# Kernel tuning notes

Measured on AMD Instinct MI355X. Metric: run time of the kernel, lower is better.

Reference implementation:

```python
import jax, jax.numpy as jnp
import numpy as np

IMG_H, IMG_W = 800, 1216
STRIDES = [4, 8, 16, 32, 64]
SIZES = [32, 64, 128, 256, 512]
RATIOS = (2.0, 1.0, 0.5)
LVTOP = 1000     # per-level top-k
IMTOP = 1000     # image-level top-k
IOU_THR = 0.7
MIN_SIZE = 0.001
BBOX_CLIP = float(np.log(1000.0 / 16.0))  # dw/dh clamp, matches decode=(1,1,log(1000/16))


def conv2d(x, w, b, pad):
    y = jax.lax.conv_general_dilated(x, w, (1, 1), [(pad, pad), (pad, pad)],
                                     dimension_numbers=('NCHW', 'OIHW', 'NCHW'))
    return y + b[None, :, None, None]


def head_level(x, conv_w, conv_b, cls_w, cls_b, reg_w, reg_b):
    # ConvUnit 3x3 + plain ReLU (no BN), then 1x1 reg/cls heads
    B = x.shape[0]
    h = jax.nn.relu(conv2d(x, conv_w, conv_b, 1))
    reg = conv2d(h, reg_w, reg_b, 0).transpose(0, 2, 3, 1).reshape(B, -1, 4)      # [B,H*W*A,4]
    scr = jax.nn.sigmoid(conv2d(h, cls_w, cls_b, 0).transpose(0, 2, 3, 1).reshape(B, -1))  # [B,H*W*A]
    return reg, scr


def make_priors(H, W, stride, size):
    # rounded base anchors (1 scale x 3 ratios), corner-aligned grid (xyxy)
    r = jnp.array(RATIOS, dtype=jnp.float32)
    hr = jnp.sqrt(r)
    ws, hs = size / hr, size * hr
    base = jnp.round(jnp.stack([-ws / 2, -hs / 2, ws / 2, hs / 2], axis=1))  # [A,4]
    ys, xs = jnp.meshgrid(jnp.arange(H) * stride, jnp.arange(W) * stride, indexing='ij')
    shift = jnp.stack([xs, ys, xs, ys], -1).reshape(-1, 1, 4).astype(jnp.float32)
    return (shift + base[None]).reshape(-1, 4)  # [H*W*A,4], order matches head reshape


def decode(reg, priors):
    pw = priors[..., 2] - priors[..., 0]
    ph = priors[..., 3] - priors[..., 1]
    pcx = priors[..., 0] + 0.5 * pw
    pcy = priors[..., 1] + 0.5 * ph
    dx, dy = reg[..., 0], reg[..., 1]
    dw = jnp.minimum(reg[..., 2], BBOX_CLIP)
    dh = jnp.minimum(reg[..., 3], BBOX_CLIP)
    cx, cy = dx * pw + pcx, dy * ph + pcy
    w, h = jnp.exp(dw) * pw, jnp.exp(dh) * ph
    return jnp.stack([cx - 0.5 * w, cy - 0.5 * h, cx + 0.5 * w, cy + 0.5 * h], -1)


def nms_keep(boxes, scores):
    # greedy NMS; boxes [K,4] sorted by score desc, scores < -0.5 mark invalid/padding
    K = boxes.shape[0]
    area = (boxes[:, 2] - boxes[:, 0]) * (boxes[:, 3] - boxes[:, 1])
    lt = jnp.maximum(boxes[:, None, :2], boxes[None, :, :2])
    rb = jnp.minimum(boxes[:, None, 2:], boxes[None, :, 2:])
    wh = jnp.clip(rb - lt, 0.0)
    inter = wh[..., 0] * wh[..., 1]
    iou = inter / jnp.maximum(area[:, None] + area[None, :] - inter, 1e-9)
    iou = jax.lax.stop_gradient(iou)  # selection is discrete
    idx = jnp.arange(K)

    def step(keep, xs):
        row, i = xs
        sup = keep[i] & (row > IOU_THR) & (idx > i)
        return keep & ~sup, None

    keep, _ = jax.lax.scan(step, scores > -0.5, (iou, idx))
    return keep


def process_level(reg, scr, priors):
    B, N = scr.shape
    k = min(LVTOP, N)
    topv, topi = jax.lax.top_k(scr, k)                              # [B,k], sorted desc
    reg_s = jnp.take_along_axis(reg, topi[..., None], axis=1)       # [B,k,4]
    boxes = decode(reg_s, priors[topi])
    boxes = jnp.stack([
        jnp.clip(boxes[..., 0], 0.0, IMG_W), jnp.clip(boxes[..., 1], 0.0, IMG_H),
        jnp.clip(boxes[..., 2], 0.0, IMG_W), jnp.clip(boxes[..., 3], 0.0, IMG_H)], -1)
    w = boxes[..., 2] - boxes[..., 0]
    h = boxes[..., 3] - boxes[..., 1]
    sc = jnp.where((w > MIN_SIZE) & (h > MIN_SIZE), topv, -1.0)     # drop tiny boxes
    if k < LVTOP:  # pad small levels (e.g. P6) to a fixed candidate count
        boxes = jnp.pad(boxes, ((0, 0), (0, LVTOP - k), (0, 0)))
        sc = jnp.pad(sc, ((0, 0), (0, LVTOP - k)), constant_values=-1.0)
    keep = jax.vmap(nms_keep)(boxes, sc)                            # per-level NMS
    return boxes, jnp.where(keep, sc, -1.0)


def forward(p2, p3, p4, p5, p6, conv_w, conv_b, cls_w, cls_b, reg_w, reg_b):
    levels = [p2, p3, p4, p5, p6]
    all_boxes, all_scores = [], []
    for lvl, stride, size in zip(levels, STRIDES, SIZES):
        reg, scr = head_level(lvl, conv_w, conv_b, cls_w, cls_b, reg_w, reg_b)
        priors = make_priors(lvl.shape[2], lvl.shape[3], stride, size)
        b, s = process_level(reg, scr, priors)
        all_boxes.append(b)
        all_scores.append(s)
    boxes = jnp.concatenate(all_boxes, axis=1)
    scores = jnp.concatenate(all_scores, axis=1)
    fv, fi = jax.lax.top_k(scores, IMTOP)                           # image-level top-k
    fb = jnp.take_along_axis(boxes, fi[..., None], axis=1)
    return jnp.concatenate([fb, fv[..., None]], axis=-1)            # [B, IMTOP, 5]


def setup_inputs():
    key = jax.random.key(0)
    ks = jax.random.split(key, 8)
    C = 256
    shapes = [(2, C, 200, 304), (2, C, 100, 152), (2, C, 50, 76), (2, C, 25, 38), (2, C, 13, 19)]
    inp = {}
    for i, (name, sh) in enumerate(zip(['p2', 'p3', 'p4', 'p5', 'p6'], shapes)):
        inp[name] = jax.random.normal(ks[i], sh, dtype=jnp.float32)
    inp['conv_w'] = jax.random.normal(ks[5], (C, C, 3, 3), dtype=jnp.float32) * 0.02
    inp['conv_b'] = jnp.zeros((C,), dtype=jnp.float32)
    inp['cls_w'] = jax.random.normal(ks[6], (3, C, 1, 1), dtype=jnp.float32) * 0.02
    inp['cls_b'] = jnp.zeros((3,), dtype=jnp.float32)
    inp['reg_w'] = jax.random.normal(ks[7], (12, C, 1, 1), dtype=jnp.float32) * 0.01
    inp['reg_b'] = jnp.zeros((12,), dtype=jnp.float32)
    return inp


def reference(p2, p3, p4, p5, p6, conv_w, conv_b, cls_w, cls_b, reg_w, reg_b):
    return forward(p2, p3, p4, p5, p6, conv_w, conv_b, cls_w, cls_b, reg_w, reg_b)
```

## Files before the change

### kernel.cpp

```cpp
#include <hip/hip_runtime.h>
#include <stdint.h>
#include <math.h>

typedef unsigned long long u64;
typedef unsigned int u32;
typedef unsigned char u8;
typedef short s16x8 __attribute__((ext_vector_type(8)));
typedef float f32x4 __attribute__((ext_vector_type(4)));

#define ATOT 242991
#define PXTOT 80997
#define PXPAD 82971

__device__ __constant__ int    d_Hs[5]      = {200,100,50,25,13};
__device__ __constant__ int    d_Ws[5]      = {304,152,76,38,19};
__device__ __constant__ int    d_Wp[5]      = {306,154,78,40,21};
__device__ __constant__ int    d_stridec[5] = {4,8,16,32,64};
__device__ __constant__ double d_sized[5]   = {32.0,64.0,128.0,256.0,512.0};
__device__ __constant__ int    d_off[5]     = {0,182400,228000,239400,242250};
__device__ __constant__ int    d_pxoff[6]   = {0,60800,76000,79800,80750,80997};
__device__ __constant__ int    d_poff[5]    = {0,61812,77520,81576,82656};
__device__ __constant__ int    d_Ncand[5]   = {182400,45600,11400,2850,741};
__device__ __constant__ int    d_xcb[5]     = {0,1900,2375,2494,2524};
__device__ __constant__ int    d_ctb[5]     = {0,1000,1300,1400,1425};
__device__ __constant__ int    d_tX[5]      = {5,3,2,1,1};
__device__ __constant__ int    d_bcum[6]    = {0,1012,1520,1776,1906,1974};

__device__ __forceinline__ u32 f2k32(float f) {
  u32 u = __float_as_uint(f);
  return (u & 0x80000000u) ? ~u : (u | 0x80000000u);
}
__device__ __forceinline__ float k2f32(u32 k) {
  u32 u = (k & 0x80000000u) ? (k & 0x7FFFFFFFu) : ~k;
  return __uint_as_float(u);
}
__device__ __forceinline__ u64 d2k(double d) {
  u64 b = (u64)__double_as_longlong(d);
  return (b & 0x8000000000000000ull) ? ~b : (b | 0x8000000000000000ull);
}
__device__ __forceinline__ unsigned short f2bf(float v) {
  u32 b = __float_as_uint(v);
  return (unsigned short)((b + 0x7FFFu + ((b >> 16) & 1u)) >> 16);
}

__global__ void wtrans_k(const float* __restrict__ w, float* __restrict__ wt) {
  int gid = blockIdx.x * 256 + threadIdx.x;
  if (gid >= 2304 * 256) return;
  int oc = gid & 255;
  int rest = gid >> 8;
  int ic = rest / 9, tap = rest % 9;
  wt[gid] = w[(oc * 256 + ic) * 9 + tap];
}

__global__ void wcvt_k(const float* __restrict__ w, short* __restrict__ wbh) {
  int gid = blockIdx.x * 256 + threadIdx.x;
  if (gid >= 73728) return;
  int lane = gid & 63;
  int rest = gid >> 6;
  int oct = rest & 15, rs = rest >> 4;
  int slice = rs & 7, tap = rs >> 3;
  int oc = oct * 16 + (lane & 15);
  int icb = slice * 32 + (lane >> 4) * 8;
  size_t ob = (size_t)gid * 8;
#pragma unroll
  for (int j = 0; j < 8; ++j)
    wbh[ob + j] = (short)f2bf(w[(oc * 256 + icb + j) * 9 + tap]);
}

__global__ void border_zero_k(short* __restrict__ xh, short* __restrict__ xl) {
  int tid = blockIdx.x * 256 + threadIdx.x;
  if (tid >= 2 * 1974 * 8) return;
  int oct = tid & 7;
  int rest = tid >> 3;
  int b = rest / 1974;
  int bi = rest % 1974;
  int lvl = 0;
#pragma unroll
  for (int l = 1; l < 5; ++l) if (bi >= d_bcum[l]) lvl = l;
  int li = bi - d_bcum[lvl];
  int W = d_Ws[lvl], H = d_Hs[lvl], Wp = d_Wp[lvl];
  int py, px;
  if (li < Wp)            { py = 0;     px = li; }
  else if (li < 2 * Wp)   { py = H + 1; px = li - Wp; }
  else { int rem = li - 2 * Wp; py = 1 + rem / 2; px = (rem & 1) ? (W + 1) : 0; }
  size_t base = ((size_t)(b * PXPAD + d_poff[lvl]) + (size_t)py * Wp + px) * 256
              + (size_t)oct * 32;
  s16x8 z = (s16x8){0,0,0,0,0,0,0,0};
#pragma unroll
  for (int j = 0; j < 4; ++j) {
    *(s16x8*)(xh + base + j * 8) = z;
    *(s16x8*)(xl + base + j * 8) = z;
  }
}

__global__ __launch_bounds__(256) void xcvt_k(
    const float* __restrict__ x0, const float* __restrict__ x1,
    const float* __restrict__ x2, const float* __restrict__ x3,
    const float* __restrict__ x4, short* __restrict__ xh, short* __restrict__ xl)
{
  __shared__ float tile[32 * 257];
  const int bid = blockIdx.x;
  const int b = bid / 2532;
  int r = bid % 2532;
  int lvl = 0;
#pragma unroll
  for (int l2 = 1; l2 < 5; ++l2) if (r >= d_xcb[l2]) lvl = l2;
  const int chunk = r - d_xcb[lvl];
  const int H = d_Hs[lvl], W = d_Ws[lvl], HW = H * W, Wp = d_Wp[lvl];
  const int px0 = chunk * 32;
  const float* xs[5] = {x0, x1, x2, x3, x4};
  const float* xb = xs[lvl] + (size_t)b * 256 * HW;
  const int t = threadIdx.x;

  for (int icg = 0; icg < 32; ++icg) {
    int ic = icg * 8 + (t >> 5);
    int px = px0 + (t & 31);
    float v = (px < HW) ? xb[(size_t)ic * HW + px] : 0.f;
    tile[(t & 31) * 257 + ic] = v;
  }
  __syncthreads();
  int px = t >> 3, sub = t & 7;
  int gpx = px0 + px;
  if (gpx < HW) {
    int yy = gpx / W, xx = gpx % W;
    size_t pxbase = ((size_t)(b * PXPAD + d_poff[lvl]) +
                     (size_t)(yy + 1) * Wp + (xx + 1)) * 256;
#pragma unroll
    for (int q = 0; q < 4; ++q) {
      int ch0 = q * 64 + sub * 8;
      s16x8 hi, lo;
#pragma unroll
      for (int j = 0; j < 8; ++j) {
        u32 bits = __float_as_uint(tile[px * 257 + ch0 + j]);
        hi[j] = (short)(bits >> 16);
        lo[j] = (short)(bits & 0xFFFFu);
      }
      *(s16x8*)(xh + pxbase + ch0) = hi;
      *(s16x8*)(xl + pxbase + ch0) = lo;
    }
  }
}

__global__ __launch_bounds__(256) void conv_mfma_k(
    const short* __restrict__ xh, const short* __restrict__ wbh,
    const float* __restrict__ convb, const float* __restrict__ clsw,
    const float* __restrict__ clsb, float* __restrict__ scr32)
{
  __shared__ float zl[4][64][3];
  const int bid = blockIdx.x;
  const int b = bid / 1438;
  int r = bid % 1438;
  int lvl = 0;
#pragma unroll
  for (int l2 = 1; l2 < 5; ++l2) if (r >= d_ctb[l2]) lvl = l2;
  const int lid = r - d_ctb[lvl];
  const int tX = d_tX[lvl];
  const int y = lid / tX, x0 = (lid % tX) * 64;
  const int W = d_Ws[lvl], Wp = d_Wp[lvl];
  const size_t pbase = (size_t)(b * PXPAD + d_poff[lvl]);

  const int t = threadIdx.x;
  const int lane = t & 63;
  const int wid = t >> 6;
  const int aoff = (lane & 15) * 256 + (lane >> 4) * 8;

  f32x4 acc[4][4];
#pragma unroll
  for (int m = 0; m < 4; ++m)
#pragma unroll
    for (int o = 0; o < 4; ++o) acc[m][o] = (f32x4){0.f, 0.f, 0.f, 0.f};

#pragma unroll 1
  for (int tap = 0; tap < 9; ++tap) {
    const int ky = tap / 3, kx = tap % 3;
    const size_t re = (pbase + (size_t)(y + ky) * Wp + (x0 + kx)) * 256;
    const short* pa = xh + re;
    const short* pbh = wbh + (size_t)tap * 8 * 16 * 512;
#pragma unroll 1
    for (int slice = 0; slice < 8; ++slice) {
      s16x8 bh[4], a[4];
#pragma unroll
      for (int o = 0; o < 4; ++o) {
        size_t bo = ((size_t)(slice * 16 + wid * 4 + o) * 64 + lane) * 8;
        bh[o] = *(const s16x8*)(pbh + bo);
      }
#pragma unroll
      for (int m = 0; m < 4; ++m) {
        size_t ao = (size_t)aoff + slice * 32 + m * 4096;
        a[m] = *(const s16x8*)(pa + ao);
      }
#pragma unroll
      for (int m = 0; m < 4; ++m)
#pragma unroll
        for (int o = 0; o < 4; ++o)
          acc[m][o] = __builtin_amdgcn_mfma_f32_16x16x32_bf16(a[m], bh[o], acc[m][o], 0, 0, 0);
    }
  }

  float bb[4], cw0[4], cw1[4], cw2[4];
#pragma unroll
  for (int o = 0; o < 4; ++o) {
    int oc = wid * 64 + o * 16 + (lane & 15);
    bb[o]  = convb[oc];
    cw0[o] = clsw[0 * 256 + oc];
    cw1[o] = clsw[1 * 256 + oc];
    cw2[o] = clsw[2 * 256 + oc];
  }
#pragma unroll
  for (int m = 0; m < 4; ++m) {
#pragma unroll
    for (int q = 0; q < 4; ++q) {
      float h0 = fmaxf(acc[m][0][q] + bb[0], 0.f);
      float h1 = fmaxf(acc[m][1][q] + bb[1], 0.f);
      float h2 = fmaxf(acc[m][2][q] + bb[2], 0.f);
      float h3 = fmaxf(acc[m][3][q] + bb[3], 0.f);
      float z0 = fmaf(h0, cw0[0], fmaf(h1, cw0[1], fmaf(h2, cw0[2], h3 * cw0[3])));
      float z1 = fmaf(h0, cw1[0], fmaf(h1, cw1[1], fmaf(h2, cw1[2], h3 * cw1[3])));
      float z2 = fmaf(h0, cw2[0], fmaf(h1, cw2[1], fmaf(h2, cw2[2], h3 * cw2[3])));
      z0 += __shfl_xor(z0, 1); z0 += __shfl_xor(z0, 2); z0 += __shfl_xor(z0, 4); z0 += __shfl_xor(z0, 8);
      z1 += __shfl_xor(z1, 1); z1 += __shfl_xor(z1, 2); z1 += __shfl_xor(z1, 4); z1 += __shfl_xor(z1, 8);
      z2 += __shfl_xor(z2, 1); z2 += __shfl_xor(z2, 2); z2 += __shfl_xor(z2, 4); z2 += __shfl_xor(z2, 8);
      if ((lane & 15) == 0) {
        int slot = m * 16 + (lane >> 4) * 4 + q;
        zl[wid][slot][0] = z0; zl[wid][slot][1] = z1; zl[wid][slot][2] = z2;
      }
    }
  }
  __syncthreads();
  if (t < 192) {
    int slot = t / 3, head = t % 3;
    int col = x0 + slot;
    if (col < W) {
      float z = zl[0][slot][head] + zl[1][slot][head] + zl[2][slot][head] +
                zl[3][slot][head] + clsb[head];
      int pix = y * W + col;
      scr32[(size_t)b * ATOT + d_off[lvl] + (size_t)pix * 3 + head] =
          1.f / (1.f + expf(-z));
    }
  }
}

__device__ __forceinline__ void locate(int gid, int& b, int& r, int& lvl) {
  b = gid / ATOT; r = gid % ATOT;
  lvl = (r < 182400) ? 0 : (r < 228000) ? 1 : (r < 239400) ? 2 : (r < 242250) ? 3 : 4;
}

__global__ void hist_hi_k(const float* __restrict__ scr, u32* __restrict__ hist) {
  int gid = blockIdx.x * 256 + threadIdx.x;
  if (gid >= 2 * ATOT) return;
  int b, r, lvl; locate(gid, b, r, lvl);
  u32 key = f2k32(scr[gid]);
  int rep = blockIdx.x & 3;
  atomicAdd(&hist[((((b * 5 + lvl) << 2) | rep) << 16) + (key >> 16)], 1u);
}

__global__ void scan_hi_k(const u32* __restrict__ hist, int* __restrict__ meta) {
  int bl = blockIdx.x, lvl = bl % 5;
  u32 k_sel = (u32)min(1000, d_Ncand[lvl]);
  const u32* h = hist + ((size_t)bl << 18);
  __shared__ u32 part[256];
  __shared__ u32 row[256];
  __shared__ int csel;
  __shared__ u32 cumsh;
  int t = threadIdx.x;
  u32 s = 0;
  for (int v = 0; v < 256; ++v) {
    int idx = t * 256 + v;
    s += h[idx] + h[65536 + idx] + h[131072 + idx] + h[196608 + idx];
  }
  part[t] = s;
  __syncthreads();
  if (t == 0) {
    u32 cum = 0; int c = 255;
    for (; c > 0; --c) { if (cum + part[c] >= k_sel) break; cum += part[c]; }
    csel = c; cumsh = cum;
  }
  __syncthreads();
  {
    int idx = csel * 256 + t;
    row[t] = h[idx] + h[65536 + idx] + h[131072 + idx] + h[196608 + idx];
  }
  __syncthreads();
  if (t == 0) {
    u32 cum = cumsh;
    int pivot = csel * 256;
    for (int v = 255; v >= 0; --v) {
      if (cum + row[v] >= k_sel) { pivot = csel * 256 + v; break; }
      cum += row[v];
    }
    meta[bl * 8 + 0] = pivot;
    meta[bl * 8 + 1] = (int)cum;
  }
}

__global__ void hist_lo_k(const float* __restrict__ scr, const int* __restrict__ meta,
                          u32* __restrict__ hist) {
  int gid = blockIdx.x * 256 + threadIdx.x;
  if (gid >= 2 * ATOT) return;
  int b, r, lvl; locate(gid, b, r, lvl);
  int bl = b * 5 + lvl;
  u32 key = f2k32(scr[gid]);
  if ((int)(key >> 16) == meta[bl * 8 + 0]) {
    int rep = blockIdx.x & 3;
    atomicAdd(&hist[(((bl << 2) | rep) << 16) + (key & 0xFFFFu)], 1u);
  }
}

__global__ void scan_lo_k(const u32* __restrict__ hist, int* __restrict__ meta) {
  int bl = blockIdx.x, lvl = bl % 5;
  u32 k_sel = (u32)min(1000, d_Ncand[lvl]);
  const u32* h = hist + ((size_t)bl << 18);
  __shared__ u32 part[256];
  __shared__ u32 row[256];
  __shared__ int csel;
  __shared__ u32 cumsh;
  int t = threadIdx.x;
  u32 s = 0;
  for (int v = 0; v < 256; ++v) {
    int idx = t * 256 + v;
    s += h[idx] + h[65536 + idx] + h[131072 + idx] + h[196608 + idx];
  }
  part[t] = s;
  __syncthreads();
  if (t == 0) {
    u32 cum = (u32)meta[bl * 8 + 1];
    int c = 255;
    for (; c > 0; --c) { if (cum + part[c] >= k_sel) break; cum += part[c]; }
    csel = c; cumsh = cum;
  }
  __syncthreads();
  {
    int idx = csel * 256 + t;
    row[t] = h[idx] + h[65536 + idx] + h[131072 + idx] + h[196608 + idx];
  }
  __syncthreads();
  if (t == 0) {
    u32 cum = cumsh;
    int pivot = csel * 256;
    for (int v = 255; v >= 0; --v) {
      if (cum + row[v] >= k_sel) { pivot = csel * 256 + v; break; }
      cum += row[v];
    }
    u32 P = (((u32)meta[bl * 8 + 0]) << 16) | (u32)pivot;
    u32 T = f2k32(k2f32(P) - 5e-3f);
    if (d_Ncand[lvl] <= 1000) T = 0;
    meta[bl * 8 + 2] = (int)T;
    meta[bl * 8 + 4] = 0;
  }
}

__global__ void compact_k(const float* __restrict__ scr, int* __restrict__ meta,
                          u32* __restrict__ complist, u8* __restrict__ flags) {
  int gid = blockIdx.x * 256 + threadIdx.x;
  if (gid >= 2 * ATOT) return;
  int b, r, lvl; locate(gid, b, r, lvl);
  int bl = b * 5 + lvl;
  u32 key = f2k32(scr[gid]);
  if (key >= (u32)meta[bl * 8 + 2]) {
    int pos = atomicAdd(&meta[bl * 8 + 4], 1);
    if (pos < 8192) {
      u32 li = (u32)(r - d_off[lvl]);
      complist[bl * 8192 + pos] = li;
      flags[b * PXTOT + d_pxoff[lvl] + li / 3] = 1;
    }
  }
}

__global__ void pxcompact_k(u8* __restrict__ flags, u32* __restrict__ worklist,
                            int* __restrict__ wlcount) {
  int gid = blockIdx.x * 256 + threadIdx.x;
  if (gid >= 2 * PXTOT) return;
  if (flags[gid]) {
    flags[gid] = 0;
    int pos = atomicAdd(wlcount, 1);
    if (pos < 65536) worklist[pos] = (u32)gid;
  }
}

#define RSG 2048
#define RSLOTS 3
__global__ __launch_bounds__(256) void rescore_k(
    const short* __restrict__ xh, const short* __restrict__ xl,
    const float* __restrict__ wt, const float* __restrict__ convb,
    const float* __restrict__ clsw, const float* __restrict__ clsb,
    const float* __restrict__ regw, const float* __restrict__ regb,
    const u32* __restrict__ worklist, const int* __restrict__ wlcount,
    double* __restrict__ scr64, double* __restrict__ reg64)
{
  __shared__ double xd[RSLOTS * 2560];
  __shared__ double hl[RSLOTS * 256];
  const int t = threadIdx.x;
  int count = *wlcount; if (count > 65536) count = 65536;

  for (int base = blockIdx.x * RSLOTS; base < count; base += RSG * RSLOTS) {
    int sb[RSLOTS], slvl[RSLOTS], spix[RSLOTS];
    size_t pb0[RSLOTS];
    bool valid[RSLOTS];
#pragma unroll
    for (int s = 0; s < RSLOTS; ++s) {
      int w = base + s;
      valid[s] = (w < count);
      sb[s] = 0; slvl[s] = 0; spix[s] = 0; pb0[s] = 0;
      if (valid[s]) {
        u32 g = worklist[w];
        int b = (int)(g / PXTOT), lp = (int)(g % PXTOT);
        int lvl = 0;
#pragma unroll
        for (int l = 1; l < 5; ++l) if (lp >= d_pxoff[l]) lvl = l;
        int pix = lp - d_pxoff[lvl];
        int W = d_Ws[lvl], Wp = d_Wp[lvl];
        int py = pix / W, px = pix % W;
        sb[s] = b; slvl[s] = lvl; spix[s] = pix;
        pb0[s] = ((size_t)(b * PXPAD + d_poff[lvl]) + (size_t)py * Wp + px) * 256;
      }
    }
    __syncthreads();
#pragma unroll
    for (int s = 0; s < RSLOTS; ++s) {
      if (valid[s]) {
        int Wp = d_Wp[slvl[s]];
        for (int i = t; i < 1152; i += 256) {
          int tap = i >> 7, pair = i & 127;
          int ky = tap / 3, kx = tap % 3;
          size_t po = pb0[s] + ((size_t)ky * Wp + kx) * 256 + (size_t)pair * 2;
          u32 vh = *(const u32*)(xh + po);
          u32 vl = *(const u32*)(xl + po);
          float xa  = __uint_as_float(((vh & 0xFFFFu) << 16) | (vl & 0xFFFFu));
          float xb2 = __uint_as_float((vh & 0xFFFF0000u) | (vl >> 16));
          xd[s * 2560 + (pair * 2) * 10 + tap]     = (double)xa;
          xd[s * 2560 + (pair * 2 + 1) * 10 + tap] = (double)xb2;
        }
      }
    }
    __syncthreads();
    double h[RSLOTS];
#pragma unroll
    for (int s = 0; s < RSLOTS; ++s) h[s] = 0.0;
    for (int ic = 0; ic < 256; ++ic) {
      double wd[9];
#pragma unroll
      for (int tap = 0; tap < 9; ++tap)
        wd[tap] = (double)wt[(ic * 9 + tap) * 256 + t];
#pragma unroll
      for (int s = 0; s < RSLOTS; ++s) {
        const double* xp = &xd[s * 2560 + ic * 10];
#pragma unroll
        for (int tap = 0; tap < 9; ++tap)
          h[s] = fma(xp[tap], wd[tap], h[s]);
      }
    }
    double bias = (double)convb[t];
#pragma unroll
    for (int s = 0; s < RSLOTS; ++s) {
      h[s] = fmax(h[s] + bias, 0.0);
      hl[s * 256 + t] = h[s];
    }
    __syncthreads();
    {
      int s = t >> 6, lane = t & 63;
      if (s < RSLOTS && valid[s]) {
        int lvl = slvl[s];
        size_t g3 = (size_t)sb[s] * ATOT + d_off[lvl] + (size_t)spix[s] * 3;
        for (int head = 0; head < 15; ++head) {
          const float* hw = (head < 3) ? (clsw + head * 256) : (regw + (head - 3) * 256);
          double part = 0.0;
#pragma unroll
          for (int q = 0; q < 4; ++q) {
            int oc = lane + q * 64;
            part = fma(hl[s * 256 + oc], (double)hw[oc], part);
          }
          part += __shfl_xor(part, 32);
          part += __shfl_xor(part, 16);
          part += __shfl_xor(part, 8);
          part += __shfl_xor(part, 4);
          part += __shfl_xor(part, 2);
          part += __shfl_xor(part, 1);
          if (lane == 0) {
            double z = part + (double)((head < 3) ? clsb[head] : regb[head - 3]);
            if (head < 3) scr64[g3 + head] = 1.0 / (1.0 + exp(-z));
            else { int hh = head - 3; reg64[(g3 + (hh >> 2)) * 4 + (hh & 3)] = z; }
          }
        }
      }
    }
    __syncthreads();
  }
}

__global__ void buildkeys_k(const u32* __restrict__ complist, const int* __restrict__ meta,
                            const double* __restrict__ scr64, u64* __restrict__ comp64) {
  int bl = blockIdx.x;
  int b = bl / 5, lvl = bl % 5;
  int M = meta[bl * 8 + 4]; if (M > 8192) M = 8192;
  for (int i = threadIdx.x; i < 8192; i += 256) {
    u64 key = 0;
    if (i < M) {
      u32 li = complist[bl * 8192 + i];
      double sc = scr64[(size_t)b * ATOT + d_off[lvl] + li];
      key = ((d2k(sc) >> 18) << 18) | (u64)(0x3FFFFu - li);
    }
    comp64[bl * 8192 + i] = key;
  }
}

__device__ void bitonic_desc_n(u64* s, int SZ) {
  int t = threadIdx.x;
  for (int k = 2; k <= SZ; k <<= 1) {
    for (int j = k >> 1; j > 0; j >>= 1) {
      __syncthreads();
      for (int i = t; i < (SZ >> 1); i += 1024) {
        int l = (i << 1) - (i & (j - 1));
        int m = l + j;
        bool up = ((l & k) == 0);
        u64 a = s[l], bb = s[m];
        if ((a < bb) == up) { s[l] = bb; s[m] = a; }
      }
    }
  }
  __syncthreads();
}

__global__ __launch_bounds__(1024) void sort_level_k(const u64* __restrict__ comp64,
                                                     const int* __restrict__ meta,
                                                     int* __restrict__ topidx) {
  int bl = blockIdx.x, lvl = bl % 5;
  int k_sel = min(1000, d_Ncand[lvl]);
  __shared__ u64 s[8192];
  int M = meta[bl * 8 + 4]; if (M > 8192) M = 8192;
  int SZ = (M <= 2048) ? 2048 : 8192;
  for (int i = threadIdx.x; i < SZ; i += 1024)
    s[i] = (i < M) ? comp64[bl * 8192 + i] : 0ull;
  __syncthreads();
  bitonic_desc_n(s, SZ);
  for (int r = threadIdx.x; r < 1000; r += 1024) {
    int v = -1;
    if (r < k_sel && r < M) v = (int)(0x3FFFFu - (u32)(s[r] & 0x3FFFFu));
    topidx[bl * 1000 + r] = v;
  }
}

__global__ void decode_k(const int* __restrict__ topidx, const double* __restrict__ scr64,
                         const double* __restrict__ reg64, double* __restrict__ boxes,
                         double* __restrict__ sc0) {
  int gid = blockIdx.x * 256 + threadIdx.x;
  if (gid >= 10000) return;
  int bl = gid / 1000, rank = gid % 1000;
  int b = bl / 5, lvl = bl % 5;
  int idx = topidx[bl * 1000 + rank];
  double X1 = 0.0, Y1 = 0.0, X2 = 0.0, Y2 = 0.0, sc = -1.0;
  if (idx >= 0) {
    size_t g = (size_t)b * ATOT + d_off[lvl] + idx;
    double s = scr64[g];
    double dx = reg64[g * 4 + 0], dy = reg64[g * 4 + 1];
    const double BCLIP = 4.135166556742356;
    double dw = fmin(reg64[g * 4 + 2], BCLIP);
    double dh = fmin(reg64[g * 4 + 3], BCLIP);
    int a = idx % 3, pix = idx / 3;
    int W = d_Ws[lvl];
    int py = pix / W, px = pix % W;
    double r = (a == 0) ? 2.0 : (a == 1) ? 1.0 : 0.5;
    double hr = sqrt(r);
    double size = d_sized[lvl];
    double wsz = size / hr, hsz = size * hr;
    double bx2 = rint(wsz * 0.5), by2 = rint(hsz * 0.5);
    double bx1 = rint(-(wsz * 0.5)), by1 = rint(-(hsz * 0.5));
    double sx = (double)(px * d_stridec[lvl]), sy = (double)(py * d_stridec[lvl]);
    double x1 = sx + bx1, yy1 = sy + by1;
    double x2 = sx + bx2, yy2 = sy + by2;
    double pw = x2 - x1, ph = yy2 - yy1;
    double pcx = x1 + 0.5 * pw, pcy = yy1 + 0.5 * ph;
    double cx = dx * pw + pcx, cy = dy * ph + pcy;
    double w = exp(dw) * pw, h = exp(dh) * ph;
    X1 = fmin(fmax(cx - 0.5 * w, 0.0), 1216.0);
    Y1 = fmin(fmax(cy - 0.5 * h, 0.0), 800.0);
    X2 = fmin(fmax(cx + 0.5 * w, 0.0), 1216.0);
    Y2 = fmin(fmax(cy + 0.5 * h, 0.0), 800.0);
    sc = ((X2 - X1) > 0.001 && (Y2 - Y1) > 0.001) ? s : -1.0;
  }
  double* bp = boxes + (size_t)(bl * 1000 + rank) * 4;
  bp[0] = X1; bp[1] = Y1; bp[2] = X2; bp[3] = Y2;
  sc0[bl * 1000 + rank] = sc;
}

__global__ __launch_bounds__(256) void nms_mask_k(const double* __restrict__ boxes,
                                                  u64* __restrict__ gmask) {
  int blk = blockIdx.x;
  int bl = blk >> 2, qt = blk & 3;
  __shared__ double X1[1000], Y1[1000], X2[1000], Y2[1000], AR[1000];
  int t = threadIdx.x;
  for (int i = t; i < 1000; i += 256) {
    const double* bp = boxes + (size_t)(bl * 1000 + i) * 4;
    double x1 = bp[0], y1 = bp[1], x2 = bp[2], y2 = bp[3];
    X1[i] = x1; Y1[i] = y1; X2[i] = x2; Y2[i] = y2;
    AR[i] = (x2 - x1) * (y2 - y1);
  }
  __syncthreads();
  if (t < 250) {
    int i = qt * 250 + t;
    double ax1 = X1[i], ay1 = Y1[i], ax2 = X2[i], ay2 = Y2[i], aa = AR[i];
    u64* gm = gmask + (size_t)bl * 16000 + (size_t)i * 16;
    for (int wj = 0; wj < 16; ++wj) {
      u64 bits = 0;
      int jb0 = wj * 64;
      for (int jb = 0; jb < 64; ++jb) {
        int j = jb0 + jb;
        if (j <= i || j >= 1000) continue;
        double lx = fmax(ax1, X1[j]), ly = fmax(ay1, Y1[j]);
        double rx = fmin(ax2, X2[j]), ry = fmin(ay2, Y2[j]);
        double ww = fmax(rx - lx, 0.0), hh = fmax(ry - ly, 0.0);
        double inter = ww * hh;
        double uni = (aa + AR[j]) - inter;
        double iou = inter / fmax(uni, 1e-9);
        if (iou > 0.7) bits |= (1ull << jb);
      }
      gm[wj] = bits;
    }
  }
}

__global__ void nms_scan_k(double* __restrict__ sc0, const u64* __restrict__ gmask) {
  int bl = blockIdx.x;
  int lane = threadIdx.x;
  const u64* gm = gmask + (size_t)bl * 16000;
  u64 keepw = 0;
  if (lane < 16) {
    for (int jb = 0; jb < 64; ++jb) {
      int j = lane * 64 + jb;
      if (j < 1000 && sc0[bl * 1000 + j] > -0.5) keepw |= (1ull << jb);
    }
  }
  u64 m0 = 0, m1 = 0, m2 = 0, m3 = 0;
  if (lane < 16) {
    m0 = gm[0 * 16 + lane]; m1 = gm[1 * 16 + lane];
    m2 = gm[2 * 16 + lane]; m3 = gm[3 * 16 + lane];
  }
  for (int i = 0; i < 1000; i += 4) {
    u64 n0 = 0, n1 = 0, n2 = 0, n3 = 0;
    if (lane < 16 && i + 4 < 1000) {
      n0 = gm[(i + 4) * 16 + lane]; n1 = gm[(i + 5) * 16 + lane];
      n2 = gm[(i + 6) * 16 + lane]; n3 = gm[(i + 7) * 16 + lane];
    }
    { u64 kw = __shfl(keepw, (i    ) >> 6); if ((kw >> ((i    ) & 63)) & 1) { if (lane < 16) keepw &= ~m0; } }
    { u64 kw = __shfl(keepw, (i + 1) >> 6); if ((kw >> ((i + 1) & 63)) & 1) { if (lane < 16) keepw &= ~m1; } }
    { u64 kw = __shfl(keepw, (i + 2) >> 6); if ((kw >> ((i + 2) & 63)) & 1) { if (lane < 16) keepw &= ~m2; } }
    { u64 kw = __shfl(keepw, (i + 3) >> 6); if ((kw >> ((i + 3) & 63)) & 1) { if (lane < 16) keepw &= ~m3; } }
    m0 = n0; m1 = n1; m2 = n2; m3 = n3;
  }
  if (lane < 16) {
    for (int jb = 0; jb < 64; ++jb) {
      int j = lane * 64 + jb;
      if (j < 1000) {
        double ss = sc0[bl * 1000 + j];
        sc0[bl * 1000 + j] = ((keepw >> jb) & 1) ? ss : -1.0;
      }
    }
  }
}

__global__ __launch_bounds__(1024) void final_k(const double* __restrict__ sc0,
                                                const double* __restrict__ boxes,
                                                float* __restrict__ out) {
  int b = blockIdx.x;
  __shared__ u64 s[8192];
  for (int i = threadIdx.x; i < 8192; i += 1024) {
    u64 v = 0;
    if (i < 5000) {
      u64 k = d2k(sc0[b * 5000 + i]);
      v = ((k >> 18) << 18) | (u64)(0x3FFFFu - (u32)i);
    }
    s[i] = v;
  }
  __syncthreads();
  bitonic_desc_n(s, 8192);
  for (int r = threadIdx.x; r < 1000; r += 1024) {
    u64 v = s[r];
    int idx = (int)(0x3FFFFu - (u32)(v & 0x3FFFFu));
    double score = sc0[b * 5000 + idx];
    const double* bp = boxes + (size_t)(b * 5000 + idx) * 4;
    float* op = out + ((size_t)b * 1000 + r) * 5;
    op[0] = (float)bp[0]; op[1] = (float)bp[1];
    op[2] = (float)bp[2]; op[3] = (float)bp[3];
    op[4] = (float)score;
  }
}

extern "C" void kernel_launch(void* const* d_in, const int* in_sizes, int n_in,
                              void* d_out, int out_size, void* d_ws, size_t ws_size,
                              hipStream_t stream) {
  const float* p[5];
  for (int i = 0; i < 5; ++i) p[i] = (const float*)d_in[i];
  const float* conv_w = (const float*)d_in[5];
  const float* conv_b = (const float*)d_in[6];
  const float* cls_w  = (const float*)d_in[7];
  const float* cls_b  = (const float*)d_in[8];
  const float* reg_w  = (const float*)d_in[9];
  const float* reg_b  = (const float*)d_in[10];
  float* out = (float*)d_out;

  char* ws = (char*)d_ws;
  size_t off = 0;
  auto alloc = [&](size_t bytes) -> void* {
    void* pt = ws + off;
    off = (off + bytes + 255) & ~(size_t)255;
    return pt;
  };
  const size_t XTB = (size_t)2 * PXPAD * 256 * 2 + 65536;
  float*  wt       = (float*) alloc(2304ull * 256 * 4);
  short*  wbh      = (short*) alloc(73728ull * 8 * 2);
  short*  xh       = (short*) alloc(XTB);
  short*  xl       = (short*) alloc(XTB);
  float*  scr32    = (float*) alloc(2ull * ATOT * 4);
  double* scr64    = (double*)alloc(2ull * ATOT * 8);
  double* reg64    = (double*)alloc(2ull * ATOT * 4 * 8);
  u32*    hist     = (u32*)   alloc(40ull * 65536 * 4);
  int*    meta     = (int*)   alloc(10ull * 8 * 4);
  u32*    complist = (u32*)   alloc(10ull * 8192 * 4);
  u64*    comp64   = (u64*)   alloc(10ull * 8192 * 8);
  u8*     flags    = (u8*)    alloc(2ull * PXTOT);
  u32*    worklist = (u32*)   alloc(65536ull * 4);
  int*    wlcount  = (int*)   alloc(256);
  int*    topidx   = (int*)   alloc(10ull * 1000 * 4);
  double* boxes    = (double*)alloc(2ull * 5000 * 4 * 8);
  double* sc0      = (double*)alloc(2ull * 5000 * 8);
  u64*    gmask    = (u64*)   alloc(10ull * 1000 * 16 * 8);

  wtrans_k<<<(2304 * 256 + 255) / 256, 256, 0, stream>>>(conv_w, wt);
  wcvt_k<<<288, 256, 0, stream>>>(conv_w, wbh);
  border_zero_k<<<(2 * 1974 * 8 + 255) / 256, 256, 0, stream>>>(xh, xl);
  xcvt_k<<<5064, 256, 0, stream>>>(p[0], p[1], p[2], p[3], p[4], xh, xl);
  conv_mfma_k<<<2876, 256, 0, stream>>>(xh, wbh, conv_b, cls_w, cls_b, scr32);

  int nblk = (2 * ATOT + 255) / 256;
  hipMemsetAsync(hist, 0, 40ull * 65536 * 4, stream);
  hist_hi_k<<<nblk, 256, 0, stream>>>(scr32, hist);
  scan_hi_k<<<10, 256, 0, stream>>>(hist, meta);
  hipMemsetAsync(hist, 0, 40ull * 65536 * 4, stream);
  hist_lo_k<<<nblk, 256, 0, stream>>>(scr32, meta, hist);
  scan_lo_k<<<10, 256, 0, stream>>>(hist, meta);

  hipMemsetAsync(flags, 0, 2ull * PXTOT, stream);
  hipMemsetAsync(wlcount, 0, 4, stream);
  compact_k<<<nblk, 256, 0, stream>>>(scr32, meta, complist, flags);
  pxcompact_k<<<(2 * PXTOT + 255) / 256, 256, 0, stream>>>(flags, worklist, wlcount);

  rescore_k<<<RSG, 256, 0, stream>>>(xh, xl, wt, conv_b, cls_w, cls_b, reg_w, reg_b,
                                     worklist, wlcount, scr64, reg64);

  buildkeys_k<<<10, 256, 0, stream>>>(complist, meta, scr64, comp64);
  sort_level_k<<<10, 1024, 0, stream>>>(comp64, meta, topidx);
  decode_k<<<40, 256, 0, stream>>>(topidx, scr64, reg64, boxes, sc0);
  nms_mask_k<<<40, 256, 0, stream>>>(boxes, gmask);
  nms_scan_k<<<10, 64, 0, stream>>>(sc0, gmask);
  final_k<<<2, 1024, 0, stream>>>(sc0, boxes, out);
}
```

Measured before the change: 1.966 ms.

## Merge prep kernels, split rescore over input-channel halves, fuse key building into sort

Combines the weight transpose, bf16 weight conversion and border zeroing into one prep launch, and folds key construction into the per-level sort kernel, removing two launches and the comp64 buffer. The fp64 rescore kernel now uses 512 threads, with each half of the block covering 128 input channels. The halves are summed through shared memory, and the input tile layout becomes tap-major so reads are contiguous across channels. This adds an extra barrier and reduction pass in exchange for more parallelism on the fp64 conv path.

After: 2.970 ms. +51.1%, slower.

```diff
diff --git a/kernel.cpp b/kernel.cpp
--- a/kernel.cpp
+++ b/kernel.cpp
@@ -43,53 +43,54 @@
   return (unsigned short)((b + 0x7FFFu + ((b >> 16) & 1u)) >> 16);
 }
 
-__global__ void wtrans_k(const float* __restrict__ w, float* __restrict__ wt) {
-  int gid = blockIdx.x * 256 + threadIdx.x;
-  if (gid >= 2304 * 256) return;
-  int oc = gid & 255;
-  int rest = gid >> 8;
-  int ic = rest / 9, tap = rest % 9;
-  wt[gid] = w[(oc * 256 + ic) * 9 + tap];
-}
-
-__global__ void wcvt_k(const float* __restrict__ w, short* __restrict__ wbh) {
-  int gid = blockIdx.x * 256 + threadIdx.x;
-  if (gid >= 73728) return;
-  int lane = gid & 63;
-  int rest = gid >> 6;
-  int oct = rest & 15, rs = rest >> 4;
-  int slice = rs & 7, tap = rs >> 3;
-  int oc = oct * 16 + (lane & 15);
-  int icb = slice * 32 + (lane >> 4) * 8;
-  size_t ob = (size_t)gid * 8;
-#pragma unroll
-  for (int j = 0; j < 8; ++j)
-    wbh[ob + j] = (short)f2bf(w[(oc * 256 + icb + j) * 9 + tap]);
-}
-
-__global__ void border_zero_k(short* __restrict__ xh, short* __restrict__ xl) {
-  int tid = blockIdx.x * 256 + threadIdx.x;
-  if (tid >= 2 * 1974 * 8) return;
-  int oct = tid & 7;
-  int rest = tid >> 3;
-  int b = rest / 1974;
-  int bi = rest % 1974;
-  int lvl = 0;
-#pragma unroll
-  for (int l = 1; l < 5; ++l) if (bi >= d_bcum[l]) lvl = l;
-  int li = bi - d_bcum[lvl];
-  int W = d_Ws[lvl], H = d_Hs[lvl], Wp = d_Wp[lvl];
-  int py, px;
-  if (li < Wp)            { py = 0;     px = li; }
-  else if (li < 2 * Wp)   { py = H + 1; px = li - Wp; }
-  else { int rem = li - 2 * Wp; py = 1 + rem / 2; px = (rem & 1) ? (W + 1) : 0; }
-  size_t base = ((size_t)(b * PXPAD + d_poff[lvl]) + (size_t)py * Wp + px) * 256
-              + (size_t)oct * 32;
-  s16x8 z = (s16x8){0,0,0,0,0,0,0,0};
-#pragma unroll
-  for (int j = 0; j < 4; ++j) {
-    *(s16x8*)(xh + base + j * 8) = z;
-    *(s16x8*)(xl + base + j * 8) = z;
+__global__ void prep_k(const float* __restrict__ w, float* __restrict__ wt,
+                       short* __restrict__ wbh, short* __restrict__ xh,
+                       short* __restrict__ xl) {
+  int blk = blockIdx.x;
+  int t = threadIdx.x;
+  if (blk < 2304) {
+    int gid = blk * 256 + t;
+    int oc = gid & 255;
+    int rest = gid >> 8;
+    int ic = rest / 9, tap = rest % 9;
+    wt[gid] = w[(oc * 256 + ic) * 9 + tap];
+  } else if (blk < 2304 + 288) {
+    int gid = (blk - 2304) * 256 + t;
+    if (gid >= 73728) return;
+    int lane = gid & 63;
+    int rest = gid >> 6;
+    int oct = rest & 15, rs = rest >> 4;
+    int slice = rs & 7, tap = rs >> 3;
+    int oc = oct * 16 + (lane & 15);
+    int icb = slice * 32 + (lane >> 4) * 8;
+    size_t ob = (size_t)gid * 8;
+#pragma unroll
+    for (int j = 0; j < 8; ++j)
+      wbh[ob + j] = (short)f2bf(w[(oc * 256 + icb + j) * 9 + tap]);
+  } else {
+    int tid = (blk - 2592) * 256 + t;
+    if (tid >= 2 * 1974 * 8) return;
+    int oct = tid & 7;
+    int rest = tid >> 3;
+    int b = rest / 1974;
+    int bi = rest % 1974;
+    int lvl = 0;
+#pragma unroll
+    for (int l = 1; l < 5; ++l) if (bi >= d_bcum[l]) lvl = l;
+    int li = bi - d_bcum[lvl];
+    int W = d_Ws[lvl], H = d_Hs[lvl], Wp = d_Wp[lvl];
+    int py, px;
+    if (li < Wp)            { py = 0;     px = li; }
+    else if (li < 2 * Wp)   { py = H + 1; px = li - Wp; }
+    else { int rem = li - 2 * Wp; py = 1 + rem / 2; px = (rem & 1) ? (W + 1) : 0; }
+    size_t base = ((size_t)(b * PXPAD + d_poff[lvl]) + (size_t)py * Wp + px) * 256
+                + (size_t)oct * 32;
+    s16x8 z = (s16x8){0,0,0,0,0,0,0,0};
+#pragma unroll
+    for (int j = 0; j < 4; ++j) {
+      *(s16x8*)(xh + base + j * 8) = z;
+      *(s16x8*)(xl + base + j * 8) = z;
+    }
   }
 }
 
@@ -379,7 +380,7 @@
 
 #define RSG 2048
 #define RSLOTS 3
-__global__ __launch_bounds__(256) void rescore_k(
+__global__ __launch_bounds__(512) void rescore_k(
     const short* __restrict__ xh, const short* __restrict__ xl,
     const float* __restrict__ wt, const float* __restrict__ convb,
     const float* __restrict__ clsw, const float* __restrict__ clsb,
@@ -387,9 +388,10 @@
     const u32* __restrict__ worklist, const int* __restrict__ wlcount,
     double* __restrict__ scr64, double* __restrict__ reg64)
 {
-  __shared__ double xd[RSLOTS * 2560];
-  __shared__ double hl[RSLOTS * 256];
+  __shared__ double xd[RSLOTS * 9 * 256];
+  __shared__ double hl[2 * RSLOTS * 256];
   const int t = threadIdx.x;
+  const int half = t >> 8, oc = t & 255;
   int count = *wlcount; if (count > 65536) count = 65536;
 
   for (int base = blockIdx.x * RSLOTS; base < count; base += RSG * RSLOTS) {
@@ -419,16 +421,16 @@
     for (int s = 0; s < RSLOTS; ++s) {
       if (valid[s]) {
         int Wp = d_Wp[slvl[s]];
-        for (int i = t; i < 1152; i += 256) {
+        for (int i = t; i < 1152; i += 512) {
           int tap = i >> 7, pair = i & 127;
           int ky = tap / 3, kx = tap % 3;
           size_t po = pb0[s] + ((size_t)ky * Wp + kx) * 256 + (size_t)pair * 2;
           u32 vh = *(const u32*)(xh + po);
           u32 vl = *(const u32*)(xl + po);
-          float xa  = __uint_as_float(((vh & 0xFFFFu) << 16) | (vl & 0xFFFFu));
-          float xb2 = __uint_as_float((vh & 0xFFFF0000u) | (vl >> 16));
-          xd[s * 2560 + (pair * 2) * 10 + tap]     = (double)xa;
-          xd[s * 2560 + (pair * 2 + 1) * 10 + tap] = (double)xb2;
+          double d0 = (double)__uint_as_float(((vh & 0xFFFFu) << 16) | (vl & 0xFFFFu));
+          double d1 = (double)__uint_as_float((vh & 0xFFFF0000u) | (vl >> 16));
+          double* dst = &xd[(s * 9 + tap) * 256 + pair * 2];
+          dst[0] = d0; dst[1] = d1;
         }
       }
     }
@@ -436,29 +438,35 @@
     double h[RSLOTS];
 #pragma unroll
     for (int s = 0; s < RSLOTS; ++s) h[s] = 0.0;
-    for (int ic = 0; ic < 256; ++ic) {
+    const int ic0 = half * 128;
+    for (int ic = ic0; ic < ic0 + 128; ++ic) {
       double wd[9];
 #pragma unroll
       for (int tap = 0; tap < 9; ++tap)
-        wd[tap] = (double)wt[(ic * 9 + tap) * 256 + t];
+        wd[tap] = (double)wt[(ic * 9 + tap) * 256 + oc];
 #pragma unroll
       for (int s = 0; s < RSLOTS; ++s) {
-        const double* xp = &xd[s * 2560 + ic * 10];
 #pragma unroll
         for (int tap = 0; tap < 9; ++tap)
-          h[s] = fma(xp[tap], wd[tap], h[s]);
-      }
-    }
-    double bias = (double)convb[t];
-#pragma unroll
-    for (int s = 0; s < RSLOTS; ++s) {
-      h[s] = fmax(h[s] + bias, 0.0);
-      hl[s * 256 + t] = h[s];
-    }
+          h[s] = fma(xd[(s * 9 + tap) * 256 + ic], wd[tap], h[s]);
+      }
+    }
+#pragma unroll
+    for (int s = 0; s < RSLOTS; ++s)
+      hl[(half * RSLOTS + s) * 256 + oc] = h[s];
     __syncthreads();
-    {
+    if (t < 256) {
+      double bias = (double)convb[t];
+#pragma unroll
+      for (int s = 0; s < RSLOTS; ++s) {
+        double v = hl[s * 256 + t] + hl[(RSLOTS + s) * 256 + t] + bias;
+        hl[s * 256 + t] = fmax(v, 0.0);
+      }
+    }
+    __syncthreads();
+    if (t < 192) {
       int s = t >> 6, lane = t & 63;
-      if (s < RSLOTS && valid[s]) {
+      if (valid[s]) {
         int lvl = slvl[s];
         size_t g3 = (size_t)sb[s] * ATOT + d_off[lvl] + (size_t)spix[s] * 3;
         for (int head = 0; head < 15; ++head) {
@@ -466,8 +474,8 @@
           double part = 0.0;
 #pragma unroll
           for (int q = 0; q < 4; ++q) {
-            int oc = lane + q * 64;
-            part = fma(hl[s * 256 + oc], (double)hw[oc], part);
+            int o2 = lane + q * 64;
+            part = fma(hl[s * 256 + o2], (double)hw[o2], part);
           }
           part += __shfl_xor(part, 32);
           part += __shfl_xor(part, 16);
@@ -487,22 +495,6 @@
   }
 }
 
-__global__ void buildkeys_k(const u32* __restrict__ complist, const int* __restrict__ meta,
-                            const double* __restrict__ scr64, u64* __restrict__ comp64) {
-  int bl = blockIdx.x;
-  int b = bl / 5, lvl = bl % 5;
-  int M = meta[bl * 8 + 4]; if (M > 8192) M = 8192;
-  for (int i = threadIdx.x; i < 8192; i += 256) {
-    u64 key = 0;
-    if (i < M) {
-      u32 li = complist[bl * 8192 + i];
-      double sc = scr64[(size_t)b * ATOT + d_off[lvl] + li];
-      key = ((d2k(sc) >> 18) << 18) | (u64)(0x3FFFFu - li);
-    }
-    comp64[bl * 8192 + i] = key;
-  }
-}
-
 __device__ void bitonic_desc_n(u64* s, int SZ) {
   int t = threadIdx.x;
   for (int k = 2; k <= SZ; k <<= 1) {
@@ -520,16 +512,25 @@
   __syncthreads();
 }
 
-__global__ __launch_bounds__(1024) void sort_level_k(const u64* __restrict__ comp64,
+__global__ __launch_bounds__(1024) void sort_level_k(const u32* __restrict__ complist,
                                                      const int* __restrict__ meta,
+                                                     const double* __restrict__ scr64,
                                                      int* __restrict__ topidx) {
   int bl = blockIdx.x, lvl = bl % 5;
+  int b = bl / 5;
   int k_sel = min(1000, d_Ncand[lvl]);
   __shared__ u64 s[8192];
   int M = meta[bl * 8 + 4]; if (M > 8192) M = 8192;
   int SZ = (M <= 2048) ? 2048 : 8192;
-  for (int i = threadIdx.x; i < SZ; i += 1024)
-    s[i] = (i < M) ? comp64[bl * 8192 + i] : 0ull;
+  for (int i = threadIdx.x; i < SZ; i += 1024) {
+    u64 key = 0;
+    if (i < M) {
+      u32 li = complist[bl * 8192 + i];
+      double sc = scr64[(size_t)b * ATOT + d_off[lvl] + li];
+      key = ((d2k(sc) >> 18) << 18) | (u64)(0x3FFFFu - li);
+    }
+    s[i] = key;
+  }
   __syncthreads();
   bitonic_desc_n(s, SZ);
   for (int r = threadIdx.x; r < 1000; r += 1024) {
@@ -715,7 +716,6 @@
   u32*    hist     = (u32*)   alloc(40ull * 65536 * 4);
   int*    meta     = (int*)   alloc(10ull * 8 * 4);
   u32*    complist = (u32*)   alloc(10ull * 8192 * 4);
-  u64*    comp64   = (u64*)   alloc(10ull * 8192 * 8);
   u8*     flags    = (u8*)    alloc(2ull * PXTOT);
   u32*    worklist = (u32*)   alloc(65536ull * 4);
   int*    wlcount  = (int*)   alloc(256);
@@ -724,9 +724,7 @@
   double* sc0      = (double*)alloc(2ull * 5000 * 8);
   u64*    gmask    = (u64*)   alloc(10ull * 1000 * 16 * 8);
 
-  wtrans_k<<<(2304 * 256 + 255) / 256, 256, 0, stream>>>(conv_w, wt);
-  wcvt_k<<<288, 256, 0, stream>>>(conv_w, wbh);
-  border_zero_k<<<(2 * 1974 * 8 + 255) / 256, 256, 0, stream>>>(xh, xl);
+  prep_k<<<2716, 256, 0, stream>>>(conv_w, wt, wbh, xh, xl);
   xcvt_k<<<5064, 256, 0, stream>>>(p[0], p[1], p[2], p[3], p[4], xh, xl);
   conv_mfma_k<<<2876, 256, 0, stream>>>(xh, wbh, conv_b, cls_w, cls_b, scr32);
 
@@ -743,11 +741,10 @@
   compact_k<<<nblk, 256, 0, stream>>>(scr32, meta, complist, flags);
   pxcompact_k<<<(2 * PXTOT + 255) / 256, 256, 0, stream>>>(flags, worklist, wlcount);
 
-  rescore_k<<<RSG, 256, 0, stream>>>(xh, xl, wt, conv_b, cls_w, cls_b, reg_w, reg_b,
+  rescore_k<<<RSG, 512, 0, stream>>>(xh, xl, wt, conv_b, cls_w, cls_b, reg_w, reg_b,
                                      worklist, wlcount, scr64, reg64);
 
-  buildkeys_k<<<10, 256, 0, stream>>>(complist, meta, scr64, comp64);
-  sort_level_k<<<10, 1024, 0, stream>>>(comp64, meta, topidx);
+  sort_level_k<<<10, 1024, 0, stream>>>(complist, meta, scr64, topidx);
   decode_k<<<40, 256, 0, stream>>>(topidx, scr64, reg64, boxes, sc0);
   nms_mask_k<<<40, 256, 0, stream>>>(boxes, gmask);
   nms_scan_k<<<10, 64, 0, stream>>>(sc0, gmask);
```
